# Kernel optimization log

Hardware: AMD Instinct MI355X
Metric: run time of the kernel (lower is better)

## Reference

```python
import jax, jax.numpy as jnp
import numpy as np

D_MODEL = 1024
N_HEADS = 16
HEAD_DIM = D_MODEL // N_HEADS
WINDOW = 256


def setup_inputs() -> dict:
    key = jax.random.key(0)
    ks = jax.random.split(key, 5)
    s = 1.0 / np.sqrt(D_MODEL)
    x = jax.random.normal(ks[0], (1, 4096, D_MODEL), dtype=jnp.float32)
    W_qkv = jax.random.uniform(ks[1], (D_MODEL, 3 * D_MODEL), jnp.float32, -s, s)
    b_qkv = jax.random.uniform(ks[2], (3 * D_MODEL,), jnp.float32, -s, s)
    W_proj = jax.random.uniform(ks[3], (D_MODEL, D_MODEL), jnp.float32, -s, s)
    b_proj = jax.random.uniform(ks[4], (D_MODEL,), jnp.float32, -s, s)
    return {"x": x, "W_qkv": W_qkv, "b_qkv": b_qkv, "W_proj": W_proj, "b_proj": b_proj}


def reference(x, W_qkv, b_qkv, W_proj, b_proj):
    b, t, c = x.shape
    qkv = x @ W_qkv + b_qkv  # [b,t,3c]
    q, k, v = jnp.split(qkv, 3, axis=-1)
    # [b,h,t,d]
    q = q.reshape(b, t, N_HEADS, HEAD_DIM).transpose(0, 2, 1, 3)
    k = k.reshape(b, t, N_HEADS, HEAD_DIM).transpose(0, 2, 1, 3)
    v = v.reshape(b, t, N_HEADS, HEAD_DIM).transpose(0, 2, 1, 3)
    att = jnp.einsum('bhqd,bhkd->bhqk', q, k) / np.sqrt(HEAD_DIM)
    idx = jnp.arange(t)
    diff = idx[:, None] - idx[None, :]  # query - key
    allowed = (diff >= 0) & (diff < WINDOW)  # causal & local window
    att = jnp.where(allowed[None, None], att, -jnp.inf)
    att = jax.nn.softmax(att, axis=-1)
    y = jnp.einsum('bhqk,bhkd->bhqd', att, v)
    y = y.transpose(0, 2, 1, 3).reshape(b, t, c)
    return y @ W_proj + b_proj
```

## Files before the change

kernel.cpp:

```cpp
#include <hip/hip_runtime.h>
#include <stdint.h>

#define TSEQ 4096
#define DMODEL 1024
#define N3 3072
#define NHEADS 16
#define HDIM 64
#define WINDOW 256

typedef __attribute__((ext_vector_type(8))) short short8;
typedef __attribute__((ext_vector_type(4))) float f32x4;

__device__ __forceinline__ unsigned short f2bf(float f) {
  unsigned u = __builtin_bit_cast(unsigned, f);
  return (unsigned short)((u + 0x7fffu + ((u >> 16) & 1u)) >> 16);
}

__device__ __forceinline__ unsigned cvtpk(float lo, float hi) {
  unsigned r;
  asm("v_cvt_pk_bf16_f32 %0, %1, %2" : "=v"(r) : "v"(lo), "v"(hi));
  return r;
}

__device__ __forceinline__ f32x4 mfma16(short8 a, short8 b, f32x4 c) {
  return __builtin_amdgcn_mfma_f32_16x16x32_bf16(a, b, c, 0, 0, 0);
}

__device__ __forceinline__ void g2lds16(const void* g, void* l) {
  __builtin_amdgcn_global_load_lds(
      (const __attribute__((address_space(1))) void*)(uintptr_t)g,
      (__attribute__((address_space(3))) void*)(uintptr_t)l,
      16, 0, 0);
}


__global__ __launch_bounds__(256) void cvt_f32_bf16_v4(const float* __restrict__ in,
                                                       unsigned short* __restrict__ out) {
  int i = (blockIdx.x * 256 + threadIdx.x) * 4;
  float4 v = *(const float4*)(in + i);
  unsigned lo = cvtpk(v.x, v.y), hi = cvtpk(v.z, v.w);
  unsigned long long packed = (unsigned long long)lo | ((unsigned long long)hi << 32);
  *(unsigned long long*)(out + i) = packed;
}

__global__ __launch_bounds__(256) void transpose_cvt2(const float* __restrict__ Wqkv,
                                                      const float* __restrict__ Wproj,
                                                      unsigned short* __restrict__ oQkvT,
                                                      unsigned short* __restrict__ oProjT) {
  __shared__ float tile[32][33];
  int bx = blockIdx.x;
  const float* in;
  unsigned short* out;
  int C;
  if (bx < 96) {
    in = Wqkv; out = oQkvT; C = N3;
  } else {
    bx -= 96; in = Wproj; out = oProjT; C = DMODEL;
  }
  const int R = DMODEL;
  int c0 = bx * 32;
  int r0 = blockIdx.y * 32;
  int tx = threadIdx.x, ty = threadIdx.y;
#pragma unroll
  for (int i = 0; i < 32; i += 8)
    tile[ty + i][tx] = in[(size_t)(r0 + ty + i) * C + c0 + tx];
  __syncthreads();
#pragma unroll
  for (int i = 0; i < 32; i += 8)
    out[(size_t)(c0 + ty + i) * R + r0 + tx] = f2bf(tile[tx][ty + i]);
}


template <int EPI>
__global__ __launch_bounds__(256)
void gemm_bf16_128(const unsigned short* __restrict__ A,
                   const unsigned short* __restrict__ BT,
                   const float* __restrict__ bias,
                   unsigned short* __restrict__ oQ,
                   unsigned short* __restrict__ oK,
                   unsigned short* __restrict__ oVT,
                   float* __restrict__ oF) {
  __shared__ unsigned short Asm[3][128 * 32];
  __shared__ unsigned short Bsm[3][128 * 32];
  const int K = 1024;
  int m0 = blockIdx.x * 128;
  int n0 = blockIdx.y * 128;
  int tid = threadIdx.x;
  int w = tid >> 6, lane = tid & 63;
  int l15 = lane & 15, l4 = lane >> 4;
  int wm = (w >> 1) * 64, wn = (w & 1) * 64;

  f32x4 acc[4][4];
#pragma unroll
  for (int i = 0; i < 4; i++)
#pragma unroll
    for (int j = 0; j < 4; j++) acc[i][j] = (f32x4){0.f, 0.f, 0.f, 0.f};

  int lr = lane >> 2;
  int slot = ((lane & 3) * 16) ^ (((lr >> 1) & 3) << 4);
  const char* aG = (const char*)(A + (size_t)(m0 + w * 32 + lr) * K) + slot;
  const char* bG = (const char*)(BT + (size_t)(n0 + w * 32 + lr) * K) + slot;
  const size_t rowSkip = (size_t)16 * K * 2;

  auto stage = [&](int s, int b) {
    int koff = s * 64;
    g2lds16(aG + koff, &Asm[b][w * 1024]);
    g2lds16(aG + rowSkip + koff, &Asm[b][w * 1024 + 512]);
    g2lds16(bG + koff, &Bsm[b][w * 1024]);
    g2lds16(bG + rowSkip + koff, &Bsm[b][w * 1024 + 512]);
  };

  int sX = ((l15 >> 1) & 3) << 4;

  auto compute = [&](int b) {
    short8 af[4], bfr[4];
#pragma unroll
    for (int mi = 0; mi < 4; mi++) {
      int rA = wm + mi * 16 + l15;
      af[mi] = *(const short8*)((const char*)Asm[b] + rA * 64 + ((l4 * 16) ^ sX));
    }
#pragma unroll
    for (int ni = 0; ni < 4; ni++) {
      int rB = wn + ni * 16 + l15;
      bfr[ni] = *(const short8*)((const char*)Bsm[b] + rB * 64 + ((l4 * 16) ^ sX));
    }
#pragma unroll
    for (int mi = 0; mi < 4; mi++)
#pragma unroll
      for (int ni = 0; ni < 4; ni++)
        acc[mi][ni] = mfma16(af[mi], bfr[ni], acc[mi][ni]);
  };

  const int NS = K / 32;
  stage(0, 0);
  stage(1, 1);
  stage(2, 2);
#pragma unroll 1
  for (int s = 0; s < NS - 2; s++) {
    asm volatile("s_waitcnt vmcnt(8)" ::: "memory");
    __builtin_amdgcn_s_barrier();
    __builtin_amdgcn_sched_barrier(0);
    compute(s % 3);
    __builtin_amdgcn_sched_barrier(0);
    __builtin_amdgcn_s_barrier();
    if (s + 3 < NS) stage(s + 3, s % 3);
  }
  asm volatile("s_waitcnt vmcnt(4)" ::: "memory");
  __builtin_amdgcn_s_barrier();
  compute((NS - 2) % 3);
  asm volatile("s_waitcnt vmcnt(0)" ::: "memory");
  __builtin_amdgcn_s_barrier();
  compute((NS - 1) % 3);

#pragma unroll
  for (int ni = 0; ni < 4; ni++) {
    int nn = n0 + wn + ni * 16 + l15;
    float bv = bias[nn];
    int c = nn & 1023;
    int hh = c >> 6, dd = c & 63;
#pragma unroll
    for (int mi = 0; mi < 4; mi++) {
      int mm = m0 + wm + mi * 16 + l4 * 4;
      float v0 = acc[mi][ni][0] + bv;
      float v1 = acc[mi][ni][1] + bv;
      float v2 = acc[mi][ni][2] + bv;
      float v3 = acc[mi][ni][3] + bv;
      if (EPI == 1) {
        oF[(size_t)(mm + 0) * 1024 + nn] = v0;
        oF[(size_t)(mm + 1) * 1024 + nn] = v1;
        oF[(size_t)(mm + 2) * 1024 + nn] = v2;
        oF[(size_t)(mm + 3) * 1024 + nn] = v3;
      } else if (nn < 1024) {
        oQ[((size_t)hh * TSEQ + mm + 0) * 64 + dd] = f2bf(v0 * 0.125f);
        oQ[((size_t)hh * TSEQ + mm + 1) * 64 + dd] = f2bf(v1 * 0.125f);
        oQ[((size_t)hh * TSEQ + mm + 2) * 64 + dd] = f2bf(v2 * 0.125f);
        oQ[((size_t)hh * TSEQ + mm + 3) * 64 + dd] = f2bf(v3 * 0.125f);
      } else if (nn < 2048) {
        oK[((size_t)hh * TSEQ + mm + 0) * 64 + dd] = f2bf(v0);
        oK[((size_t)hh * TSEQ + mm + 1) * 64 + dd] = f2bf(v1);
        oK[((size_t)hh * TSEQ + mm + 2) * 64 + dd] = f2bf(v2);
        oK[((size_t)hh * TSEQ + mm + 3) * 64 + dd] = f2bf(v3);
      } else {
        unsigned lo = cvtpk(v0, v1), hi = cvtpk(v2, v3);
        unsigned long long pv = (unsigned long long)lo | ((unsigned long long)hi << 32);
        *(unsigned long long*)(oVT + ((size_t)hh * 64 + dd) * TSEQ + mm) = pv;
      }
    }
  }
}


__global__ __launch_bounds__(256)
void attn_swa(const unsigned short* __restrict__ Qa,
              const unsigned short* __restrict__ Ka,
              const unsigned short* __restrict__ Vt,
              unsigned short* __restrict__ Y) {
  __shared__ __align__(16) char KV[2][16384];
  __shared__ __align__(16) unsigned char Pl[4][2048];
  int flat = blockIdx.x;
  int swz = (flat & 7) * 128 + (flat >> 3);
  int h = swz >> 6, qb = swz & 63;
  int w = threadIdx.x >> 6, lane = threadIdx.x & 63;
  int l15 = lane & 15, l4 = lane >> 4;
  int qrow0 = qb * 64 + w * 16;
  int q = qrow0 + l15;

  const unsigned short* qp = Qa + ((size_t)h * TSEQ + q) * 64 + l4 * 8;
  short8 qf0 = *(const short8*)qp;
  short8 qf1 = *(const short8*)(qp + 32);

  const char* kgb = (const char*)(Ka + (size_t)h * TSEQ * 64);
  const char* vgb = (const char*)(Vt + (size_t)h * 64 * TSEQ);

  auto stage = [&](int kt, int b) {
    int kbase = kt * 64;
    int sub = lane >> 3, slot = (lane & 7) * 16;
    if (w < 2) {
      int R0 = w * 32;
      const char* src = kgb + (size_t)kbase * 128;
#pragma unroll
      for (int j = 0; j < 4; j++) {
        int r = R0 + j * 8 + sub;
        g2lds16(src + r * 128 + (slot ^ ((r & 7) << 4)), &KV[b][R0 * 128 + j * 1024]);
      }
    } else {
      int D0 = (w - 2) * 32;
      const char* src = vgb + (size_t)kbase * 2;
#pragma unroll
      for (int j = 0; j < 4; j++) {
        int d = D0 + j * 8 + sub;
        g2lds16(src + (size_t)d * 8192 + (slot ^ ((d & 7) << 4)),
                &KV[b][8192 + D0 * 128 + j * 1024]);
      }
    }
  };

  float m = -1e30f, lsum = 0.f;
  f32x4 o[4];
#pragma unroll
  for (int ni = 0; ni < 4; ni++) o[ni] = (f32x4){0.f, 0.f, 0.f, 0.f};

  unsigned char* pw = Pl[w];
  int xw = (l15 & 7) << 4;

  auto compute = [&](int kt, int b, int MODE) {
    int kbase = kt * 64;
    const char* kb = KV[b];
    const char* vb = KV[b] + 8192;
    f32x4 s[4];
#pragma unroll
    for (int ni = 0; ni < 4; ni++) {
      int rb = (ni * 16 + l15) * 128;
      short8 k0 = *(const short8*)(kb + rb + ((l4 * 16) ^ xw));
      short8 k1 = *(const short8*)(kb + rb + ((64 + l4 * 16) ^ xw));
      f32x4 z = (f32x4){0.f, 0.f, 0.f, 0.f};
      z = mfma16(k0, qf0, z);
      s[ni] = mfma16(k1, qf1, z);
    }
    if (MODE != 0) {
#pragma unroll
      for (int ni = 0; ni < 4; ni++)
#pragma unroll
        for (int r = 0; r < 4; r++) {
          int key = kbase + ni * 16 + l4 * 4 + r;
          bool ok = (MODE == 2) ? (key <= q) : (q - key < WINDOW);
          s[ni][r] = ok ? s[ni][r] : -1e30f;
        }
    }
    float pm0 = fmaxf(fmaxf(s[0][0], s[0][1]), fmaxf(s[0][2], s[0][3]));
    float pm1 = fmaxf(fmaxf(s[1][0], s[1][1]), fmaxf(s[1][2], s[1][3]));
    float pm2 = fmaxf(fmaxf(s[2][0], s[2][1]), fmaxf(s[2][2], s[2][3]));
    float pm3 = fmaxf(fmaxf(s[3][0], s[3][1]), fmaxf(s[3][2], s[3][3]));
    float pm = fmaxf(fmaxf(pm0, pm1), fmaxf(pm2, pm3));
    pm = fmaxf(pm, __shfl_xor(pm, 16, 64));
    pm = fmaxf(pm, __shfl_xor(pm, 32, 64));
    float mn = fmaxf(m, pm);
    float alpha = __expf(m - mn);
    m = mn;
    float rs = 0.f;
#pragma unroll
    for (int ni = 0; ni < 4; ni++)
#pragma unroll
      for (int r = 0; r < 4; r++) {
        float p = __expf(s[ni][r] - mn);
        s[ni][r] = p;
        rs += p;
      }
    rs += __shfl_xor(rs, 16, 64);
    rs += __shfl_xor(rs, 32, 64);
    lsum = lsum * alpha + rs;
#pragma unroll
    for (int ni = 0; ni < 4; ni++) {
      unsigned lo = cvtpk(s[ni][0], s[ni][1]);
      unsigned hi = cvtpk(s[ni][2], s[ni][3]);
      unsigned long long pv = (unsigned long long)lo | ((unsigned long long)hi << 32);
      *(unsigned long long*)(pw + l15 * 128 + ((ni * 32 + l4 * 8) ^ xw)) = pv;
    }
    short8 pa0 = *(const short8*)(pw + l15 * 128 + ((l4 * 16) ^ xw));
    short8 pa1 = *(const short8*)(pw + l15 * 128 + ((64 + l4 * 16) ^ xw));
#pragma unroll
    for (int ni = 0; ni < 4; ni++)
#pragma unroll
      for (int r = 0; r < 4; r++) o[ni][r] *= alpha;
#pragma unroll
    for (int ni = 0; ni < 4; ni++) {
      int rb = (ni * 16 + l15) * 128;
      short8 v0 = *(const short8*)(vb + rb + ((l4 * 16) ^ xw));
      short8 v1 = *(const short8*)(vb + rb + ((64 + l4 * 16) ^ xw));
      o[ni] = mfma16(v0, pa0, o[ni]);
      o[ni] = mfma16(v1, pa1, o[ni]);
    }
  };

  int kt0 = qb >= 4 ? qb - 4 : 0;
  int NT = qb - kt0 + 1;
  stage(kt0, 0);
  for (int t = 0; t < NT; t++) {
    int kt = kt0 + t;
    if (t + 1 < NT) {
      stage(kt + 1, (t + 1) & 1);
      asm volatile("s_waitcnt vmcnt(4)" ::: "memory");
    } else {
      asm volatile("s_waitcnt vmcnt(0)" ::: "memory");
    }
    __builtin_amdgcn_s_barrier();
    __builtin_amdgcn_sched_barrier(0);
    int MODE = (t == NT - 1) ? 2 : ((qb >= 4 && t == 0) ? 1 : 0);
    compute(kt, t & 1, MODE);
    __builtin_amdgcn_sched_barrier(0);
    __builtin_amdgcn_s_barrier();
  }

  float inv = 1.f / lsum;
#pragma unroll
  for (int ni = 0; ni < 4; ni++) {
    unsigned lo = cvtpk(o[ni][0] * inv, o[ni][1] * inv);
    unsigned hi = cvtpk(o[ni][2] * inv, o[ni][3] * inv);
    unsigned long long yv = (unsigned long long)lo | ((unsigned long long)hi << 32);
    *(unsigned long long*)(Y + (size_t)q * DMODEL + h * 64 + ni * 16 + l4 * 4) = yv;
  }
}


extern "C" void kernel_launch(void* const* d_in, const int* in_sizes, int n_in,
                              void* d_out, int out_size, void* d_ws, size_t ws_size,
                              hipStream_t stream) {
  const float* x = (const float*)d_in[0];
  const float* Wqkv = (const float*)d_in[1];
  const float* bqkv = (const float*)d_in[2];
  const float* Wproj = (const float*)d_in[3];
  const float* bproj = (const float*)d_in[4];
  float* out = (float*)d_out;

  unsigned short* ws = (unsigned short*)d_ws;
  unsigned short* xb = ws;
  unsigned short* wqkvT = xb + (size_t)TSEQ * DMODEL;
  unsigned short* wprojT = wqkvT + (size_t)N3 * DMODEL;
  unsigned short* qarr = wprojT + (size_t)DMODEL * DMODEL;
  unsigned short* karr = qarr + (size_t)NHEADS * TSEQ * HDIM;
  unsigned short* vtarr = karr + (size_t)NHEADS * TSEQ * HDIM;
  unsigned short* yarr = vtarr + (size_t)NHEADS * TSEQ * HDIM;

  cvt_f32_bf16_v4<<<(TSEQ * DMODEL) / 1024, 256, 0, stream>>>(x, xb);
  transpose_cvt2<<<dim3(128, 32), dim3(32, 8), 0, stream>>>(Wqkv, Wproj, wqkvT, wprojT);
  gemm_bf16_128<0><<<dim3(TSEQ / 128, N3 / 128), 256, 0, stream>>>(xb, wqkvT, bqkv, qarr, karr, vtarr, nullptr);
  attn_swa<<<1024, 256, 0, stream>>>(qarr, karr, vtarr, yarr);
  gemm_bf16_128<1><<<dim3(TSEQ / 128, DMODEL / 128), 256, 0, stream>>>(yarr, wprojT, bproj, nullptr, nullptr, nullptr, out);
}
```

Measured before the change: 89.05 us.

## Use 128x64 tiles for projection GEMM and restructure to single-barrier pipeline

```diff
diff --git a/kernel.cpp b/kernel.cpp
--- a/kernel.cpp
+++ b/kernel.cpp
@@ -71,7 +71,7 @@
 }
 
 
-template <int EPI>
+template <int EPI, int NI>
 __global__ __launch_bounds__(256)
 void gemm_bf16_128(const unsigned short* __restrict__ A,
                    const unsigned short* __restrict__ BT,
@@ -80,80 +80,86 @@
                    unsigned short* __restrict__ oK,
                    unsigned short* __restrict__ oVT,
                    float* __restrict__ oF) {
+  constexpr int BN = NI * 32;
   __shared__ unsigned short Asm[3][128 * 32];
-  __shared__ unsigned short Bsm[3][128 * 32];
+  __shared__ unsigned short Bsm[3][BN * 32];
   const int K = 1024;
   int m0 = blockIdx.x * 128;
-  int n0 = blockIdx.y * 128;
+  int n0 = blockIdx.y * BN;
   int tid = threadIdx.x;
   int w = tid >> 6, lane = tid & 63;
   int l15 = lane & 15, l4 = lane >> 4;
-  int wm = (w >> 1) * 64, wn = (w & 1) * 64;
-
-  f32x4 acc[4][4];
+  int wm = (w >> 1) * 64, wn = (w & 1) * (NI * 16);
+
+  f32x4 acc[4][NI];
 #pragma unroll
   for (int i = 0; i < 4; i++)
 #pragma unroll
-    for (int j = 0; j < 4; j++) acc[i][j] = (f32x4){0.f, 0.f, 0.f, 0.f};
+    for (int j = 0; j < NI; j++) acc[i][j] = (f32x4){0.f, 0.f, 0.f, 0.f};
 
   int lr = lane >> 2;
   int slot = ((lane & 3) * 16) ^ (((lr >> 1) & 3) << 4);
   const char* aG = (const char*)(A + (size_t)(m0 + w * 32 + lr) * K) + slot;
-  const char* bG = (const char*)(BT + (size_t)(n0 + w * 32 + lr) * K) + slot;
   const size_t rowSkip = (size_t)16 * K * 2;
+  const char* bG;
+  if constexpr (NI == 4) {
+    bG = (const char*)(BT + (size_t)(n0 + w * 32 + lr) * K) + slot;
+  } else {
+    bG = (const char*)(BT + (size_t)(n0 + w * 16 + lr) * K) + slot;
+  }
 
   auto stage = [&](int s, int b) {
     int koff = s * 64;
     g2lds16(aG + koff, &Asm[b][w * 1024]);
     g2lds16(aG + rowSkip + koff, &Asm[b][w * 1024 + 512]);
-    g2lds16(bG + koff, &Bsm[b][w * 1024]);
-    g2lds16(bG + rowSkip + koff, &Bsm[b][w * 1024 + 512]);
+    if constexpr (NI == 4) {
+      g2lds16(bG + koff, &Bsm[b][w * 1024]);
+      g2lds16(bG + rowSkip + koff, &Bsm[b][w * 1024 + 512]);
+    } else {
+      g2lds16(bG + koff, &Bsm[b][w * 512]);
+    }
   };
 
   int sX = ((l15 >> 1) & 3) << 4;
 
   auto compute = [&](int b) {
-    short8 af[4], bfr[4];
+    short8 af[4], bfr[NI];
 #pragma unroll
     for (int mi = 0; mi < 4; mi++) {
       int rA = wm + mi * 16 + l15;
       af[mi] = *(const short8*)((const char*)Asm[b] + rA * 64 + ((l4 * 16) ^ sX));
     }
 #pragma unroll
-    for (int ni = 0; ni < 4; ni++) {
+    for (int ni = 0; ni < NI; ni++) {
       int rB = wn + ni * 16 + l15;
       bfr[ni] = *(const short8*)((const char*)Bsm[b] + rB * 64 + ((l4 * 16) ^ sX));
     }
 #pragma unroll
     for (int mi = 0; mi < 4; mi++)
 #pragma unroll
-      for (int ni = 0; ni < 4; ni++)
+      for (int ni = 0; ni < NI; ni++)
         acc[mi][ni] = mfma16(af[mi], bfr[ni], acc[mi][ni]);
   };
 
   const int NS = K / 32;
   stage(0, 0);
   stage(1, 1);
-  stage(2, 2);
 #pragma unroll 1
-  for (int s = 0; s < NS - 2; s++) {
-    asm volatile("s_waitcnt vmcnt(8)" ::: "memory");
+  for (int s = 0; s < NS - 1; s++) {
+    if constexpr (NI == 4) asm volatile("s_waitcnt vmcnt(4)" ::: "memory");
+    else                   asm volatile("s_waitcnt vmcnt(3)" ::: "memory");
     __builtin_amdgcn_s_barrier();
     __builtin_amdgcn_sched_barrier(0);
+    if (s + 2 < NS) stage(s + 2, (s + 2) % 3);
     compute(s % 3);
-    __builtin_amdgcn_sched_barrier(0);
-    __builtin_amdgcn_s_barrier();
-    if (s + 3 < NS) stage(s + 3, s % 3);
-  }
-  asm volatile("s_waitcnt vmcnt(4)" ::: "memory");
-  __builtin_amdgcn_s_barrier();
-  compute((NS - 2) % 3);
+  }
   asm volatile("s_waitcnt vmcnt(0)" ::: "memory");
   __builtin_amdgcn_s_barrier();
+  __builtin_amdgcn_sched_barrier(0);
   compute((NS - 1) % 3);
 
 #pragma unroll
-  for (int ni = 0; ni < 4; ni++) {
+  for (int ni = 0; ni < NI; ni++) {
     int nn = n0 + wn + ni * 16 + l15;
     float bv = bias[nn];
     int c = nn & 1023;
@@ -363,7 +369,7 @@
 
   cvt_f32_bf16_v4<<<(TSEQ * DMODEL) / 1024, 256, 0, stream>>>(x, xb);
   transpose_cvt2<<<dim3(128, 32), dim3(32, 8), 0, stream>>>(Wqkv, Wproj, wqkvT, wprojT);
-  gemm_bf16_128<0><<<dim3(TSEQ / 128, N3 / 128), 256, 0, stream>>>(xb, wqkvT, bqkv, qarr, karr, vtarr, nullptr);
+  gemm_bf16_128<0, 4><<<dim3(TSEQ / 128, N3 / 128), 256, 0, stream>>>(xb, wqkvT, bqkv, qarr, karr, vtarr, nullptr);
   attn_swa<<<1024, 256, 0, stream>>>(qarr, karr, vtarr, yarr);
-  gemm_bf16_128<1><<<dim3(TSEQ / 128, DMODEL / 128), 256, 0, stream>>>(yarr, wprojT, bproj, nullptr, nullptr, nullptr, out);
-}
+  gemm_bf16_128<1, 2><<<dim3(TSEQ / 128, DMODEL / 64), 256, 0, stream>>>(yarr, wprojT, bproj, nullptr, nullptr, nullptr, out);
+}
```

After: 85.84 us. 1.04x faster.
